# Kernel optimization log

Measured on AMD Instinct MI355X. Metric: run time of the kernel, lower is better.

The kernel has to match this reference:

```python
import jax, jax.numpy as jnp
import numpy as np

DIM = 512
NHEADS = 8
HEAD_DIM = DIM // NHEADS
LN_EPS = 1e-5


def _layernorm(x, g, b):
    m = jnp.mean(x, axis=-1, keepdims=True)
    v = jnp.mean((x - m) ** 2, axis=-1, keepdims=True)
    return (x - m) * jax.lax.rsqrt(v + LN_EPS) * g + b


def setup_inputs() -> dict:
    key = jax.random.key(0)
    ks = jax.random.split(key, 12)
    s = 1.0 / np.sqrt(DIM)
    inp = {
        "x": jax.random.normal(ks[0], (4, 2048, DIM), dtype=jnp.float32),
        "Wq": jax.random.uniform(ks[1], (DIM, DIM), jnp.float32, -s, s),
        "bq": jnp.zeros((DIM,), jnp.float32),
        "Wk": jax.random.uniform(ks[2], (DIM, DIM), jnp.float32, -s, s),
        "bk": jnp.zeros((DIM,), jnp.float32),
        "Wv": jax.random.uniform(ks[3], (DIM, DIM), jnp.float32, -s, s),
        "bv": jnp.zeros((DIM,), jnp.float32),
        "Wo": jax.random.uniform(ks[4], (DIM, DIM), jnp.float32, -s, s),
        "bo": jnp.zeros((DIM,), jnp.float32),
        "W1": jax.random.uniform(ks[5], (DIM, 2 * DIM), jnp.float32, -s, s),
        "b1": jnp.zeros((2 * DIM,), jnp.float32),
        "W2": jax.random.uniform(ks[6], (2 * DIM, DIM), jnp.float32, -1.0 / np.sqrt(2 * DIM), 1.0 / np.sqrt(2 * DIM)),
        "b2": jnp.zeros((DIM,), jnp.float32),
        "g1": jnp.ones((DIM,), jnp.float32),
        "be1": jnp.zeros((DIM,), jnp.float32),
        "g2": jnp.ones((DIM,), jnp.float32),
        "be2": jnp.zeros((DIM,), jnp.float32),
    }
    return inp


def reference(x, Wq, bq, Wk, bk, Wv, bv, Wo, bo, W1, b1, W2, b2, g1, be1, g2, be2):
    # norm_before=True path; dropout disabled (inference)
    bsz, n, _ = x.shape
    res = x
    xn = _layernorm(x, g1, be1)

    def proj(W, b):
        return (xn @ W + b).reshape(bsz, n, NHEADS, HEAD_DIM).transpose(0, 2, 1, 3)  # (B,H,N,D)

    q = proj(Wq, bq) / np.sqrt(HEAD_DIM).astype(np.float32)
    k = proj(Wk, bk)
    v = proj(Wv, bv)

    q = jax.nn.elu(q) + 1.0
    k = jax.nn.elu(k) + 1.0

    # quadratic score as in the original module (B,H,N,N)
    score = jnp.einsum("bhnd,bhmd->bhnm", q, k)
    denom = jnp.sum(score, axis=-1, keepdims=True) + 1e-5
    score = score / denom
    out = jnp.einsum("bhnm,bhmd->bhnd", score, v)

    out = out.transpose(0, 2, 1, 3).reshape(bsz, n, DIM)
    out = out @ Wo + bo
    out = res + out

    res2 = out
    h = _layernorm(out, g2, be2)
    h = jax.nn.relu(h @ W1 + b1) @ W2 + b2
    return res2 + h
```

## Files before the change

kernel.cpp:

```cpp
#include <hip/hip_runtime.h>
#include <hip/hip_bf16.h>
#include <math.h>

#define DIM 512
#define HEADS 8
#define HD 64
#define ROWS_TOTAL 8192
#define SEQ 2048
#define NSLICE 16

typedef __hip_bfloat16 bf16;
typedef __bf16 bf16x8 __attribute__((ext_vector_type(8)));
typedef float f32x4 __attribute__((ext_vector_type(4)));

__device__ __forceinline__ float elu1(float x) {
    return x > 0.f ? x + 1.f : __expf(x);
}
__device__ __forceinline__ void gl16(const void* g, void* l) {
    __builtin_amdgcn_global_load_lds(
        (const __attribute__((address_space(1))) void*)g,
        (__attribute__((address_space(3))) void*)l, 16, 0, 0);
}
__device__ __forceinline__ unsigned short f2bu(float v) {
    bf16 t = __float2bfloat16(v);
    return *(unsigned short*)&t;
}

__global__ __launch_bounds__(256) void prep_kernel(
    const float* __restrict__ Wq, const float* __restrict__ Wk,
    const float* __restrict__ Wv, const float* __restrict__ Wo,
    const float* __restrict__ W1, const float* __restrict__ W2,
    bf16* WqkvT, bf16* WoT, bf16* W1T, bf16* W2T,
    const float* __restrict__ x, const float* __restrict__ g,
    const float* __restrict__ b, bf16* __restrict__ xout,
    bf16* __restrict__ xb)
{
    __shared__ float t[32][33];
    int bx = blockIdx.x;
    if (bx >= 2048) {
        int row  = (bx - 2048) * 4 + (threadIdx.x >> 6);
        int lane = threadIdx.x & 63;
        const float* xr = x + (size_t)row * DIM + lane * 8;
        float4 v1 = *(const float4*)xr;
        float4 v2 = *(const float4*)(xr + 4);
        float f[8] = {v1.x, v1.y, v1.z, v1.w, v2.x, v2.y, v2.z, v2.w};
        int c = lane * 8;
        bf16 rb[8];
#pragma unroll
        for (int j = 0; j < 8; ++j) rb[j] = __float2bfloat16(f[j]);
        *(uint4*)(xb + (size_t)row * DIM + c) = *(uint4*)rb;
        float s = 0.f, sq = 0.f;
#pragma unroll
        for (int j = 0; j < 8; ++j) { s += f[j]; sq += f[j]*f[j]; }
#pragma unroll
        for (int off = 32; off > 0; off >>= 1) {
            s  += __shfl_xor(s,  off, 64);
            sq += __shfl_xor(sq, off, 64);
        }
        float mean = s * (1.f / DIM);
        float var  = sq * (1.f / DIM) - mean * mean;
        float rstd = rsqrtf(var + 1e-5f);
        float4 ga = *(const float4*)(g + c);
        float4 gb = *(const float4*)(g + c + 4);
        float4 ba = *(const float4*)(b + c);
        float4 bb = *(const float4*)(b + c + 4);
        float gg[8]  = {ga.x,ga.y,ga.z,ga.w,gb.x,gb.y,gb.z,gb.w};
        float bbv[8] = {ba.x,ba.y,ba.z,ba.w,bb.x,bb.y,bb.z,bb.w};
        bf16 ob[8];
#pragma unroll
        for (int j = 0; j < 8; ++j)
            ob[j] = __float2bfloat16((f[j] - mean) * rstd * gg[j] + bbv[j]);
        *(uint4*)(xout + (size_t)row * DIM + c) = *(uint4*)ob;
        return;
    }
    const float* W; bf16* T; int K, N, tk, tn, mode = 0;
    if (bx < 1024) {
        int m = bx >> 8, tix = bx & 255;
        const float* ws_[4] = {Wq, Wk, Wv, Wo};
        W = ws_[m];
        T = (m == 3) ? WoT : WqkvT;
        mode = (m == 1) ? 1 : (m == 2 ? 2 : 0);
        K = 512; N = 512; tn = tix & 15; tk = tix >> 4;
    } else if (bx < 1536) {
        int tix = bx - 1024; W = W1; T = W1T; K = 512; N = 1024; tn = tix & 31; tk = tix >> 5;
    } else {
        int tix = bx - 1536; W = W2; T = W2T; K = 1024; N = 512; tn = tix & 15; tk = tix >> 4;
    }
    int n0 = tn * 32, k0 = tk * 32;
    int tx = threadIdx.x & 31, ty = threadIdx.x >> 5;
#pragma unroll
    for (int i = 0; i < 32; i += 8)
        t[ty + i][tx] = W[(size_t)(k0 + ty + i) * N + n0 + tx];
    __syncthreads();
#pragma unroll
    for (int i = 0; i < 32; i += 8) {
        int n = n0 + ty + i;
        int dr = n;
        if (mode == 1)      dr = 512 + ((n >> 6) << 7) + (n & 63);
        else if (mode == 2) dr = 576 + ((n >> 6) << 7) + (n & 63);
        T[(size_t)dr * K + k0 + tx] = __float2bfloat16(t[tx][ty + i]);
    }
}

__global__ __launch_bounds__(256) void ln_kernel(const bf16* __restrict__ xv,
                                                 const float* __restrict__ g,
                                                 const float* __restrict__ b,
                                                 bf16* __restrict__ out)
{
    int row  = blockIdx.x * 4 + (threadIdx.x >> 6);
    int lane = threadIdx.x & 63;
    bf16x8 v = *(const bf16x8*)(xv + (size_t)row * DIM + lane * 8);
    float f[8];
#pragma unroll
    for (int j = 0; j < 8; ++j) f[j] = (float)v[j];
    float s = 0.f, sq = 0.f;
#pragma unroll
    for (int j = 0; j < 8; ++j) { s += f[j]; sq += f[j]*f[j]; }
#pragma unroll
    for (int off = 32; off > 0; off >>= 1) {
        s  += __shfl_xor(s,  off, 64);
        sq += __shfl_xor(sq, off, 64);
    }
    float mean = s * (1.f / DIM);
    float var  = sq * (1.f / DIM) - mean * mean;
    float rstd = rsqrtf(var + 1e-5f);
    int c = lane * 8;
    float4 ga = *(const float4*)(g + c);
    float4 gb = *(const float4*)(g + c + 4);
    float4 ba = *(const float4*)(b + c);
    float4 bb = *(const float4*)(b + c + 4);
    float gg[8]  = {ga.x,ga.y,ga.z,ga.w,gb.x,gb.y,gb.z,gb.w};
    float bbv[8] = {ba.x,ba.y,ba.z,ba.w,bb.x,bb.y,bb.z,bb.w};
    bf16 ob[8];
#pragma unroll
    for (int j = 0; j < 8; ++j)
        ob[j] = __float2bfloat16((f[j] - mean) * rstd * gg[j] + bbv[j]);
    *(uint4*)(out + (size_t)row * DIM + c) = *(uint4*)ob;
}

__global__ __launch_bounds__(256) void qkv_kv_kernel(
    const bf16* __restrict__ A, const bf16* __restrict__ Bt,
    const float* __restrict__ bq, const float* __restrict__ bk,
    const float* __restrict__ bv, bf16* __restrict__ Qb,
    bf16* __restrict__ KVTp, float* __restrict__ KSp, float scale)
{
    constexpr int K = 512;
    __shared__ __align__(16) bf16 SH[16384];
    int tid = threadIdx.x;
    int lane = tid & 63, wid = tid >> 6;
    int wr = wid >> 1, wc = wid & 1;
    int cpx = gridDim.x >> 3;
    int work = (blockIdx.x & 7) * cpx + (blockIdx.x >> 3);
    int bx = work % 12, by = work / 12;
    int m0 = by * 128, n0 = bx * 128;
    int sr = tid >> 2, sc = (tid & 3) * 8;
    const bf16* ga = A  + (size_t)(m0 + sr) * K + sc;
    const bf16* gb = Bt + (size_t)(n0 + sr) * K + sc;
    f32x4 acc[4][4] = {};
    int la = lane & 15, ka = lane >> 4;

    {
        gl16(ga, &SH[tid * 8]);
        gl16(ga + (size_t)64 * K, &SH[tid * 8 + 2048]);
        gl16(gb, &SH[8192 + tid * 8]);
        gl16(gb + (size_t)64 * K, &SH[8192 + tid * 8 + 2048]);
    }
    __syncthreads();
    for (int t = 0; t < 16; ++t) {
        int cur = t & 1;
        if (t + 1 < 16) {
            int k0 = (t + 1) << 5;
            bf16* As_ = SH + (cur ^ 1) * 4096;
            bf16* Bs_ = SH + 8192 + (cur ^ 1) * 4096;
            gl16(ga + k0, &As_[tid * 8]);
            gl16(ga + (size_t)64 * K + k0, &As_[tid * 8 + 2048]);
            gl16(gb + k0, &Bs_[tid * 8]);
            gl16(gb + (size_t)64 * K + k0, &Bs_[tid * 8 + 2048]);
        }
        const bf16* As_ = SH + cur * 4096;
        const bf16* Bs_ = SH + 8192 + cur * 4096;
        bf16x8 a[4], b[4];
#pragma unroll
        for (int m = 0; m < 4; ++m)
            a[m] = *(const bf16x8*)&As_[(wr * 64 + m * 16 + la) * 32 + ka * 8];
#pragma unroll
        for (int n = 0; n < 4; ++n)
            b[n] = *(const bf16x8*)&Bs_[(wc * 64 + n * 16 + la) * 32 + ka * 8];
#pragma unroll
        for (int m = 0; m < 4; ++m)
#pragma unroll
            for (int n = 0; n < 4; ++n)
                acc[m][n] = __builtin_amdgcn_mfma_f32_16x16x32_bf16(a[m], b[n], acc[m][n], 0, 0, 0);
        __syncthreads();
    }

    int rg = (lane >> 4) * 4;
    if (bx < 4) {
#pragma unroll
        for (int m = 0; m < 4; ++m) {
            int gm = m0 + wr * 64 + m * 16 + rg;
#pragma unroll
            for (int n = 0; n < 4; ++n) {
                int gnl = bx * 128 + wc * 64 + n * 16 + la;
                float bv_ = bq[gnl];
#pragma unroll
                for (int j = 0; j < 4; ++j) {
                    float v = elu1((acc[m][n][j] + bv_) * scale);
                    Qb[(size_t)(gm + j) * 512 + gnl] = __float2bfloat16(v);
                }
            }
        }
    } else {
        int hh = bx - 4;
        int bb = m0 >> 11, sl = (m0 >> 7) & 15;
        int bh = bb * 8 + hh;
        bf16* KT = SH;
        bf16* VT = SH + 8192;
        const float* bias = (wc == 0) ? (bk + hh * 64) : (bv + hh * 64);
        bf16* base = (wc == 0) ? KT : VT;
#pragma unroll
        for (int m = 0; m < 4; ++m) {
            int r0 = wr * 64 + m * 16 + rg;
#pragma unroll
            for (int n = 0; n < 4; ++n) {
                int col = n * 16 + la;
                float bv_ = bias[col];
                ushort4 pk;
                unsigned short* pp = (unsigned short*)&pk;
#pragma unroll
                for (int j = 0; j < 4; ++j) {
                    float v = acc[m][n][j] + bv_;
                    if (wc == 0) v = elu1(v);
                    pp[j] = f2bu(v);
                }
                int byteoff = col * 256 + ((r0 * 2) ^ ((col & 7) << 4));
                *(ushort4*)((char*)base + byteoff) = pk;
            }
        }
        __syncthreads();
        f32x4 acc2[4] = {};
        int fe = wid;
#pragma unroll
        for (int kk = 0; kk < 4; ++kk) {
            int kbyte = kk * 64 + ka * 16;
            int ar = fe * 16 + la;
            bf16x8 av = *(const bf16x8*)((char*)VT + ar * 256 + (kbyte ^ ((ar & 7) << 4)));
#pragma unroll
            for (int fd = 0; fd < 4; ++fd) {
                int br = fd * 16 + la;
                bf16x8 bk8 = *(const bf16x8*)((char*)KT + br * 256 + (kbyte ^ ((br & 7) << 4)));
                acc2[fd] = __builtin_amdgcn_mfma_f32_16x16x32_bf16(av, bk8, acc2[fd], 0, 0, 0);
            }
        }
        bf16* dst = KVTp + (size_t)(bh * 16 + sl) * 4096;
#pragma unroll
        for (int fd = 0; fd < 4; ++fd)
#pragma unroll
            for (int j = 0; j < 4; ++j)
                dst[(fe * 16 + rg + j) * 64 + fd * 16 + la] = __float2bfloat16(acc2[fd][j]);
        if (tid < 64) {
            float s = 0.f;
#pragma unroll
            for (int rc = 0; rc < 16; ++rc) {
                bf16x8 kv8 = *(const bf16x8*)((char*)KT + tid * 256 + ((rc * 16) ^ ((tid & 7) << 4)));
#pragma unroll
                for (int j = 0; j < 8; ++j) s += (float)kv8[j];
            }
            KSp[(size_t)(bh * 16 + sl) * 64 + tid] = s;
        }
    }
}

template<int BM, int BN, int EPI>
__global__ __launch_bounds__(256) void mfma_gemm(
    const bf16* __restrict__ A, const bf16* __restrict__ Bt,
    const float* __restrict__ b0, const bf16* __restrict__ resid,
    void* __restrict__ O0, int N, int K, int GX)
{
    constexpr int MW = BM / 32;
    constexpr int NW = BN / 32;
    __shared__ __align__(16) bf16 As[2][BM * 64];
    __shared__ __align__(16) bf16 Bs[2][BN * 64];
    int tid = threadIdx.x;
    int lane = tid & 63, wid = tid >> 6;
    int wr = wid >> 1, wc = wid & 1;
    int cpx = gridDim.x >> 3;
    int work = (blockIdx.x & 7) * cpx + (blockIdx.x >> 3);
    int bx = work % GX, by = work / GX;
    int m0 = by * BM, n0 = bx * BN;
    int sr = tid >> 3;
    int scb = (((tid & 7) << 4) ^ ((sr & 7) << 4)) >> 1;
    const bf16* ga = A  + (size_t)(m0 + sr) * K + scb;
    const bf16* gb = Bt + (size_t)(n0 + sr) * K + scb;
    f32x4 acc[MW][NW] = {};
    int la = lane & 15, ka = lane >> 4;
    int xo = (la & 7) << 4;
    int nt = K >> 6;

#pragma unroll
    for (int j = 0; j < MW; ++j)
        gl16(ga + (size_t)j * 32 * K, &As[0][tid * 8 + j * 2048]);
#pragma unroll
    for (int j = 0; j < NW; ++j)
        gl16(gb + (size_t)j * 32 * K, &Bs[0][tid * 8 + j * 2048]);
    __syncthreads();

    for (int t = 0; t < nt; ++t) {
        int cur = t & 1;
        if (t + 1 < nt) {
            int k0 = (t + 1) << 6;
#pragma unroll
            for (int j = 0; j < MW; ++j)
                gl16(ga + (size_t)j * 32 * K + k0, &As[cur ^ 1][tid * 8 + j * 2048]);
#pragma unroll
            for (int j = 0; j < NW; ++j)
                gl16(gb + (size_t)j * 32 * K + k0, &Bs[cur ^ 1][tid * 8 + j * 2048]);
        }
        const char* Ab = (const char*)As[cur];
        const char* Bb = (const char*)Bs[cur];
        bf16x8 a[2][MW], b[2][NW];
#pragma unroll
        for (int kk = 0; kk < 2; ++kk) {
            int kb = (kk * 64 + ka * 16) ^ xo;
#pragma unroll
            for (int m = 0; m < MW; ++m)
                a[kk][m] = *(const bf16x8*)(Ab + (wr * (BM/2) + m * 16 + la) * 128 + kb);
#pragma unroll
            for (int n = 0; n < NW; ++n)
                b[kk][n] = *(const bf16x8*)(Bb + (wc * (BN/2) + n * 16 + la) * 128 + kb);
        }
#pragma unroll
        for (int kk = 0; kk < 2; ++kk)
#pragma unroll
            for (int m = 0; m < MW; ++m)
#pragma unroll
                for (int n = 0; n < NW; ++n)
                    acc[m][n] = __builtin_amdgcn_mfma_f32_16x16x32_bf16(a[kk][m], b[kk][n], acc[m][n], 0, 0, 0);
        __syncthreads();
    }

    int rg = (lane >> 4) * 4;
#pragma unroll
    for (int m = 0; m < MW; ++m) {
        int gm = m0 + wr * (BM/2) + m * 16 + rg;
#pragma unroll
        for (int n = 0; n < NW; ++n) {
            int gn = n0 + wc * (BN/2) + n * 16 + la;
            float bv_ = b0[gn];
#pragma unroll
            for (int j = 0; j < 4; ++j) {
                float v = acc[m][n][j] + bv_;
                if (EPI == 3) v = fmaxf(v, 0.f);
                if ((EPI == 0 || EPI == 2) && resid)
                    v += (float)resid[(size_t)(gm + j) * N + gn];
                if (EPI == 0) ((float*)O0)[(size_t)(gm + j) * N + gn] = v;
                else          ((bf16*)O0)[(size_t)(gm + j) * N + gn] = __float2bfloat16(v);
            }
        }
    }
}

__global__ __launch_bounds__(256) void attn_gemm(
    const bf16* __restrict__ Q, const bf16* __restrict__ KVTp,
    const float* __restrict__ KSp, bf16* __restrict__ out)
{
    __shared__ __align__(16) bf16 As[128][72];
    __shared__ __align__(16) bf16 Bs[64][72];
    __shared__ float ks[64];
    __shared__ float dn[128];
    int h = blockIdx.x;
    int m0 = blockIdx.y * 128;
    int bh = ((m0 >> 11) << 3) + h;
    int tid = threadIdx.x;
    int lane = tid & 63, wid = tid >> 6;
    {
        int r = tid >> 3, c0 = (tid & 7) * 8;
#pragma unroll
        for (int p = 0; p < 4; ++p) {
            int row = p * 32 + r;
            *(bf16x8*)&As[row][c0] =
                *(const bf16x8*)(Q + (size_t)(m0 + row) * DIM + h * HD + c0);
        }
        const bf16* kvb = KVTp + (size_t)bh * 16 * 4096;
        int e = tid & 63, d0 = (tid >> 6) * 16;
        float s_[16] = {};
#pragma unroll
        for (int sl = 0; sl < NSLICE; ++sl) {
            const bf16* p = kvb + sl * 4096 + e * 64 + d0;
            bf16x8 u0 = *(const bf16x8*)p;
            bf16x8 u1 = *(const bf16x8*)(p + 8);
#pragma unroll
            for (int i = 0; i < 8; ++i) { s_[i] += (float)u0[i]; s_[8 + i] += (float)u1[i]; }
        }
#pragma unroll
        for (int i = 0; i < 16; ++i)
            Bs[e][d0 + i] = __float2bfloat16(s_[i]);
        if (tid < 64) {
            float s = 0.f;
#pragma unroll
            for (int sl = 0; sl < NSLICE; ++sl)
                s += KSp[(size_t)(bh * 16 + sl) * 64 + tid];
            ks[tid] = s;
        }
    }
    __syncthreads();
    if (tid < 128) {
        float s = 0.f;
#pragma unroll
        for (int c = 0; c < 8; ++c) {
            bf16x8 qv = *(const bf16x8*)&As[tid][c * 8];
#pragma unroll
            for (int j = 0; j < 8; ++j)
                s += (float)qv[j] * ks[c * 8 + j];
        }
        dn[tid] = 1.f / (s + 1e-5f);
    }
    int la = lane & 15, ka = lane >> 4;
    f32x4 acc[2][4] = {};
#pragma unroll
    for (int s = 0; s < 2; ++s) {
        bf16x8 a[2], b[4];
#pragma unroll
        for (int m = 0; m < 2; ++m)
            a[m] = *(const bf16x8*)&As[wid * 32 + m * 16 + la][s * 32 + ka * 8];
#pragma unroll
        for (int n = 0; n < 4; ++n)
            b[n] = *(const bf16x8*)&Bs[n * 16 + la][s * 32 + ka * 8];
#pragma unroll
        for (int m = 0; m < 2; ++m)
#pragma unroll
            for (int n = 0; n < 4; ++n)
                acc[m][n] = __builtin_amdgcn_mfma_f32_16x16x32_bf16(a[m], b[n], acc[m][n], 0, 0, 0);
    }
    __syncthreads();
    int rg = (lane >> 4) * 4;
#pragma unroll
    for (int m = 0; m < 2; ++m) {
#pragma unroll
        for (int j = 0; j < 4; ++j) {
            int lr = wid * 32 + m * 16 + rg + j;
            float rdn = dn[lr];
            int gm = m0 + lr;
#pragma unroll
            for (int n = 0; n < 4; ++n) {
                int gn = h * HD + n * 16 + la;
                out[(size_t)gm * DIM + gn] = __float2bfloat16(acc[m][n][j] * rdn);
            }
        }
    }
}

extern "C" void kernel_launch(void* const* d_in, const int* in_sizes, int n_in,
                              void* d_out, int out_size, void* d_ws, size_t ws_size,
                              hipStream_t stream)
{
    const float* x   = (const float*)d_in[0];
    const float* Wq  = (const float*)d_in[1];
    const float* bq  = (const float*)d_in[2];
    const float* Wk  = (const float*)d_in[3];
    const float* bk  = (const float*)d_in[4];
    const float* Wv  = (const float*)d_in[5];
    const float* bv  = (const float*)d_in[6];
    const float* Wo  = (const float*)d_in[7];
    const float* bo  = (const float*)d_in[8];
    const float* W1  = (const float*)d_in[9];
    const float* b1  = (const float*)d_in[10];
    const float* W2  = (const float*)d_in[11];
    const float* b2  = (const float*)d_in[12];
    const float* g1  = (const float*)d_in[13];
    const float* be1 = (const float*)d_in[14];
    const float* g2  = (const float*)d_in[15];
    const float* be2 = (const float*)d_in[16];

    char* wsb = (char*)d_ws;
    const size_t MB = 1u << 20;
    bf16*  Qb  = (bf16*)(wsb + 0 * MB);
    bf16*  xn  = (bf16*)(wsb + 8 * MB);
    bf16*  yb  = (bf16*)(wsb + 16 * MB);
    bf16*  hb  = (bf16*)(wsb + 24 * MB);
    bf16*  WqkvT = (bf16*)(wsb + 32 * MB);
    bf16*  WoT = WqkvT + 1536 * 512;
    bf16*  W1T = WoT + 512 * 512;
    bf16*  W2T = W1T + 1024 * 512;
    bf16*  KVTp = (bf16*)(wsb + 40 * MB);
    float* KSp  = (float*)(wsb + 44 * MB);
    bf16*  xb   = (bf16*)(wsb + 45 * MB);
    bf16*  F1  = (bf16*)(wsb + 0 * MB);
    bf16*  attnb = xn;

    float* out = (float*)d_out;
    dim3 blk(256);

    prep_kernel<<<4096, blk, 0, stream>>>(Wq, Wk, Wv, Wo, W1, W2,
                                          WqkvT, WoT, W1T, W2T, x, g1, be1, xn, xb);
    qkv_kv_kernel<<<768, blk, 0, stream>>>(xn, WqkvT, bq, bk, bv,
                                           Qb, KVTp, KSp, 0.125f);
    attn_gemm<<<dim3(8, 64), blk, 0, stream>>>(Qb, KVTp, KSp, attnb);
    mfma_gemm<64, 64, 2><<<1024, blk, 0, stream>>>(
        attnb, WoT, bo, xb, yb, 512, 512, 8);
    ln_kernel<<<2048, blk, 0, stream>>>(yb, g2, be2, hb);
    mfma_gemm<64, 64, 3><<<2048, blk, 0, stream>>>(
        hb, W1T, b1, nullptr, F1, 1024, 512, 16);
    mfma_gemm<64, 64, 0><<<1024, blk, 0, stream>>>(
        F1, W2T, b2, yb, out, 512, 1024, 8);
}
```

Baseline: 112.0 us.

## Overlap Wo/W1/W2 transposes with attention and read fp32 residual directly

```diff
diff --git a/kernel.cpp b/kernel.cpp
--- a/kernel.cpp
+++ b/kernel.cpp
@@ -26,29 +26,42 @@
     return *(unsigned short*)&t;
 }
 
+__device__ __forceinline__ void wt_tile(const float* W, bf16* T, int K, int N,
+                                        int tk, int tn, int mode, int tid,
+                                        float (*t)[33])
+{
+    int n0 = tn * 32, k0 = tk * 32;
+    int tx = tid & 31, ty = tid >> 5;
+#pragma unroll
+    for (int i = 0; i < 32; i += 8)
+        t[ty + i][tx] = W[(size_t)(k0 + ty + i) * N + n0 + tx];
+    __syncthreads();
+#pragma unroll
+    for (int i = 0; i < 32; i += 8) {
+        int n = n0 + ty + i;
+        int dr = n;
+        if (mode == 1)      dr = 512 + ((n >> 6) << 7) + (n & 63);
+        else if (mode == 2) dr = 576 + ((n >> 6) << 7) + (n & 63);
+        T[(size_t)dr * K + k0 + tx] = __float2bfloat16(t[tx][ty + i]);
+    }
+}
+
 __global__ __launch_bounds__(256) void prep_kernel(
     const float* __restrict__ Wq, const float* __restrict__ Wk,
-    const float* __restrict__ Wv, const float* __restrict__ Wo,
-    const float* __restrict__ W1, const float* __restrict__ W2,
-    bf16* WqkvT, bf16* WoT, bf16* W1T, bf16* W2T,
+    const float* __restrict__ Wv, bf16* WqkvT,
     const float* __restrict__ x, const float* __restrict__ g,
-    const float* __restrict__ b, bf16* __restrict__ xout,
-    bf16* __restrict__ xb)
+    const float* __restrict__ b, bf16* __restrict__ xout)
 {
     __shared__ float t[32][33];
     int bx = blockIdx.x;
-    if (bx >= 2048) {
-        int row  = (bx - 2048) * 4 + (threadIdx.x >> 6);
+    if (bx < 2048) {
+        int row  = bx * 4 + (threadIdx.x >> 6);
         int lane = threadIdx.x & 63;
         const float* xr = x + (size_t)row * DIM + lane * 8;
         float4 v1 = *(const float4*)xr;
         float4 v2 = *(const float4*)(xr + 4);
         float f[8] = {v1.x, v1.y, v1.z, v1.w, v2.x, v2.y, v2.z, v2.w};
         int c = lane * 8;
-        bf16 rb[8];
-#pragma unroll
-        for (int j = 0; j < 8; ++j) rb[j] = __float2bfloat16(f[j]);
-        *(uint4*)(xb + (size_t)row * DIM + c) = *(uint4*)rb;
         float s = 0.f, sq = 0.f;
 #pragma unroll
         for (int j = 0; j < 8; ++j) { s += f[j]; sq += f[j]*f[j]; }
@@ -73,33 +86,10 @@
         *(uint4*)(xout + (size_t)row * DIM + c) = *(uint4*)ob;
         return;
     }
-    const float* W; bf16* T; int K, N, tk, tn, mode = 0;
-    if (bx < 1024) {
-        int m = bx >> 8, tix = bx & 255;
-        const float* ws_[4] = {Wq, Wk, Wv, Wo};
-        W = ws_[m];
-        T = (m == 3) ? WoT : WqkvT;
-        mode = (m == 1) ? 1 : (m == 2 ? 2 : 0);
-        K = 512; N = 512; tn = tix & 15; tk = tix >> 4;
-    } else if (bx < 1536) {
-        int tix = bx - 1024; W = W1; T = W1T; K = 512; N = 1024; tn = tix & 31; tk = tix >> 5;
-    } else {
-        int tix = bx - 1536; W = W2; T = W2T; K = 1024; N = 512; tn = tix & 15; tk = tix >> 4;
-    }
-    int n0 = tn * 32, k0 = tk * 32;
-    int tx = threadIdx.x & 31, ty = threadIdx.x >> 5;
-#pragma unroll
-    for (int i = 0; i < 32; i += 8)
-        t[ty + i][tx] = W[(size_t)(k0 + ty + i) * N + n0 + tx];
-    __syncthreads();
-#pragma unroll
-    for (int i = 0; i < 32; i += 8) {
-        int n = n0 + ty + i;
-        int dr = n;
-        if (mode == 1)      dr = 512 + ((n >> 6) << 7) + (n & 63);
-        else if (mode == 2) dr = 576 + ((n >> 6) << 7) + (n & 63);
-        T[(size_t)dr * K + k0 + tx] = __float2bfloat16(t[tx][ty + i]);
-    }
+    int tix = bx - 2048;
+    int m = tix >> 8, sub = tix & 255;
+    const float* ws_[3] = {Wq, Wk, Wv};
+    wt_tile(ws_[m], WqkvT, 512, 512, sub >> 4, sub & 15, m, threadIdx.x, t);
 }
 
 __global__ __launch_bounds__(256) void ln_kernel(const bf16* __restrict__ xv,
@@ -274,7 +264,7 @@
 template<int BM, int BN, int EPI>
 __global__ __launch_bounds__(256) void mfma_gemm(
     const bf16* __restrict__ A, const bf16* __restrict__ Bt,
-    const float* __restrict__ b0, const bf16* __restrict__ resid,
+    const float* __restrict__ b0, const void* __restrict__ resid,
     void* __restrict__ O0, int N, int K, int GX)
 {
     constexpr int MW = BM / 32;
@@ -351,8 +341,10 @@
             for (int j = 0; j < 4; ++j) {
                 float v = acc[m][n][j] + bv_;
                 if (EPI == 3) v = fmaxf(v, 0.f);
-                if ((EPI == 0 || EPI == 2) && resid)
-                    v += (float)resid[(size_t)(gm + j) * N + gn];
+                if (EPI == 0 && resid)
+                    v += (float)((const bf16*)resid)[(size_t)(gm + j) * N + gn];
+                if (EPI == 4 && resid)
+                    v += ((const float*)resid)[(size_t)(gm + j) * N + gn];
                 if (EPI == 0) ((float*)O0)[(size_t)(gm + j) * N + gn] = v;
                 else          ((bf16*)O0)[(size_t)(gm + j) * N + gn] = __float2bfloat16(v);
             }
@@ -360,18 +352,36 @@
     }
 }
 
-__global__ __launch_bounds__(256) void attn_gemm(
+__global__ __launch_bounds__(256) void attn_plus_kernel(
     const bf16* __restrict__ Q, const bf16* __restrict__ KVTp,
-    const float* __restrict__ KSp, bf16* __restrict__ out)
+    const float* __restrict__ KSp, bf16* __restrict__ out,
+    const float* __restrict__ Wo, const float* __restrict__ W1,
+    const float* __restrict__ W2,
+    bf16* WoT, bf16* W1T, bf16* W2T)
 {
     __shared__ __align__(16) bf16 As[128][72];
     __shared__ __align__(16) bf16 Bs[64][72];
     __shared__ float ks[64];
     __shared__ float dn[128];
-    int h = blockIdx.x;
-    int m0 = blockIdx.y * 128;
+    int bid = blockIdx.x;
+    int tid = threadIdx.x;
+    if (bid >= 512) {
+        float (*t)[33] = (float(*)[33])As;
+        int tix = bid - 512;
+        if (tix < 256)
+            wt_tile(Wo, WoT, 512, 512, tix >> 4, tix & 15, 0, tid, t);
+        else if (tix < 768) {
+            int u = tix - 256;
+            wt_tile(W1, W1T, 512, 1024, u >> 5, u & 31, 0, tid, t);
+        } else {
+            int u = tix - 768;
+            wt_tile(W2, W2T, 1024, 512, u >> 4, u & 15, 0, tid, t);
+        }
+        return;
+    }
+    int h = bid & 7;
+    int m0 = (bid >> 3) * 128;
     int bh = ((m0 >> 11) << 3) + h;
-    int tid = threadIdx.x;
     int lane = tid & 63, wid = tid >> 6;
     {
         int r = tid >> 3, c0 = (tid & 7) * 8;
@@ -484,20 +494,19 @@
     bf16*  W2T = W1T + 1024 * 512;
     bf16*  KVTp = (bf16*)(wsb + 40 * MB);
     float* KSp  = (float*)(wsb + 44 * MB);
-    bf16*  xb   = (bf16*)(wsb + 45 * MB);
     bf16*  F1  = (bf16*)(wsb + 0 * MB);
     bf16*  attnb = xn;
 
     float* out = (float*)d_out;
     dim3 blk(256);
 
-    prep_kernel<<<4096, blk, 0, stream>>>(Wq, Wk, Wv, Wo, W1, W2,
-                                          WqkvT, WoT, W1T, W2T, x, g1, be1, xn, xb);
+    prep_kernel<<<2816, blk, 0, stream>>>(Wq, Wk, Wv, WqkvT, x, g1, be1, xn);
     qkv_kv_kernel<<<768, blk, 0, stream>>>(xn, WqkvT, bq, bk, bv,
                                            Qb, KVTp, KSp, 0.125f);
-    attn_gemm<<<dim3(8, 64), blk, 0, stream>>>(Qb, KVTp, KSp, attnb);
-    mfma_gemm<64, 64, 2><<<1024, blk, 0, stream>>>(
-        attnb, WoT, bo, xb, yb, 512, 512, 8);
+    attn_plus_kernel<<<1792, blk, 0, stream>>>(Qb, KVTp, KSp, attnb,
+                                               Wo, W1, W2, WoT, W1T, W2T);
+    mfma_gemm<64, 64, 4><<<1024, blk, 0, stream>>>(
+        attnb, WoT, bo, x, yb, 512, 512, 8);
     ln_kernel<<<2048, blk, 0, stream>>>(yb, g2, be2, hb);
     mfma_gemm<64, 64, 3><<<2048, blk, 0, stream>>>(
         hb, W1T, b1, nullptr, F1, 1024, 512, 16);
```

Measured after the change: 112.1 us. Within noise of the previous version (+0.1%).
